# Kernel tuning notes

Measured on AMD Instinct MI355X. Metric: run time of the kernel, lower is better.

Reference implementation:

```python
import jax, jax.numpy as jnp
import numpy as np

NU, NI, K, D, B = 100000, 50000, 100, 64, 8192


def setup_inputs() -> dict:
    key = jax.random.key(0)
    ks = jax.random.split(key, 16)
    s = lambda fan_in: np.sqrt(2.0 / fan_in)  # kaiming_normal-ish scale
    return {
        "user_emb": jax.random.normal(ks[0], (NU, D), jnp.float32) * s(D),
        "item_emb": jax.random.normal(ks[1], (NI, D), jnp.float32) * s(D),
        "user_scr_tensor": jax.random.uniform(ks[2], (NU, K), jnp.float32) / K,
        "item_scr_tensor": jax.random.uniform(ks[3], (NI, K), jnp.float32) / K,
        "w1": jax.random.normal(ks[4], (64, 128), jnp.float32) * s(128),
        "b1": jnp.zeros((64,), jnp.float32),
        "w2": jax.random.normal(ks[5], (64, 64), jnp.float32) * s(64),
        "b2": jnp.zeros((64,), jnp.float32),
        "w3": jax.random.normal(ks[6], (32, 64), jnp.float32) * s(64),
        "b3": jnp.zeros((32,), jnp.float32),
        "w4": jax.random.normal(ks[7], (32, 32), jnp.float32) * s(32),
        "b4": jnp.zeros((32,), jnp.float32),
        "w5": jax.random.normal(ks[8], (1, 32), jnp.float32) * s(32),
        "b5": jnp.zeros((1,), jnp.float32),
        "user_idx_tensor": jax.random.randint(ks[9], (NU, K), 0, NU, jnp.int32),
        "item_idx_tensor": jax.random.randint(ks[10], (NI, K), 0, NI, jnp.int32),
        "user_idxs": jax.random.randint(ks[11], (B,), 0, NU, jnp.int32),
        "item_idxs": jax.random.randint(ks[12], (B,), 0, NI, jnp.int32),
    }


def _scored_pool(idx_tensor, emb, scr, idxs):
    neighs = idx_tensor[idxs]          # [B, K]
    neigh_emb = emb[neighs]            # [B, K, D]
    neigh_scr = scr[neighs]            # [B, K, K]
    return jnp.einsum("bkj,bjd->bkd", neigh_scr, neigh_emb)


def reference(user_emb, item_emb, user_scr_tensor, item_scr_tensor,
              w1, b1, w2, b2, w3, b3, w4, b4, w5, b5,
              user_idx_tensor, item_idx_tensor, user_idxs, item_idxs):
    su = _scored_pool(user_idx_tensor, user_emb, user_scr_tensor, user_idxs)  # [B,K,D]
    si = _scored_pool(item_idx_tensor, item_emb, item_scr_tensor, item_idxs)  # [B,K,D]
    x = jnp.concatenate([su, si], axis=2)  # [B, K, 2D]
    x = jax.nn.relu(x @ w1.T + b1)
    x = jax.nn.relu(x @ w2.T + b2)
    x = jax.nn.relu(x @ w3.T + b3)
    x = jax.nn.relu(x @ w4.T + b4)
    x = jax.nn.sigmoid(x @ w5.T + b5)  # [B, K, 1]
    return jnp.mean(x, axis=-2).squeeze()  # [B]
```

## Files before the change

### kernel.cpp

```cpp
#include <hip/hip_runtime.h>
#include <hip/hip_bf16.h>
#include <math.h>

typedef __attribute__((ext_vector_type(8))) short short8;
typedef __attribute__((ext_vector_type(4))) float f32x4;

#define KN 100

#define W1_OFF 0
#define W2_OFF 8192
#define W3_OFF 12288
#define W4_OFF 14336
#define SCRU_OFF 16384
#define SCRI_OFF (SCRU_OFF + 100000 * 128)
#define EMBU_OFF (SCRI_OFF + 50000 * 128)
#define EMBI_OFF (EMBU_OFF + 100000 * 64)
#define NB_OFF   (EMBI_OFF + 50000 * 64)

#define ETU 0
#define ETI 8704
#define XU  17408
#define XI  8704
#define S_TOT 25472

__device__ __forceinline__ unsigned short f2bf(float f) {
  __hip_bfloat16 h = __float2bfloat16(f);
  return __builtin_bit_cast(unsigned short, h);
}

__device__ __forceinline__ void st8(unsigned short* d, float4 a, float4 b) {
  short8 h;
  h[0] = (short)f2bf(a.x); h[1] = (short)f2bf(a.y);
  h[2] = (short)f2bf(a.z); h[3] = (short)f2bf(a.w);
  h[4] = (short)f2bf(b.x); h[5] = (short)f2bf(b.y);
  h[6] = (short)f2bf(b.z); h[7] = (short)f2bf(b.w);
  *reinterpret_cast<short8*>(d) = h;
}

__global__ void prep(const float* __restrict__ w1, const float* __restrict__ w2,
                     const float* __restrict__ w3, const float* __restrict__ w4,
                     const float* __restrict__ uscr, const float* __restrict__ iscr,
                     const float* __restrict__ uemb, const float* __restrict__ iemb,
                     const int* __restrict__ uidx_t, const int* __restrict__ iidx_t,
                     const int* __restrict__ uidxs, const int* __restrict__ iidxs,
                     unsigned short* __restrict__ ws) {
  int t = blockIdx.x * 256 + threadIdx.x;
  if (t < 15360) {
    const float* src; int rel, o, i, kt, base;
    if (t < 8192)       { src = w1; rel = t;         o = rel >> 7; i = rel & 127; kt = 4; base = W1_OFF; }
    else if (t < 12288) { src = w2; rel = t - 8192;  o = rel >> 6; i = rel & 63;  kt = 2; base = W2_OFF; }
    else if (t < 14336) { src = w3; rel = t - 12288; o = rel >> 6; i = rel & 63;  kt = 2; base = W3_OFF; }
    else                { src = w4; rel = t - 14336; o = rel >> 5; i = rel & 31;  kt = 1; base = W4_OFF; }
    int n = o >> 4, l15 = o & 15, k = i >> 5, quad = (i >> 3) & 3, j = i & 7;
    ws[base + ((n * kt + k) * 64 + quad * 16 + l15) * 8 + j] = f2bf(src[rel]);
    return;
  }
  int rel = t - 15360;
  const float4 z4 = {0.f, 0.f, 0.f, 0.f};
  if (rel < 2400000) {
    const float* src; unsigned short* dst; int row, g;
    if (rel < 1600000) {
      row = rel >> 4; g = rel & 15;
      src = uscr + (size_t)row * 100;
      dst = ws + SCRU_OFF + (size_t)row * 128 + g * 8;
    } else {
      int q = rel - 1600000; row = q >> 4; g = q & 15;
      src = iscr + (size_t)row * 100;
      dst = ws + SCRI_OFF + (size_t)row * 128 + g * 8;
    }
    float4 va = (g < 13) ? *reinterpret_cast<const float4*>(src + g * 8) : z4;
    float4 vb = (g < 12) ? *reinterpret_cast<const float4*>(src + g * 8 + 4) : z4;
    st8(dst, va, vb);
    return;
  }
  rel -= 2400000;
  if (rel < 1200000) {
    const float* src; unsigned short* dst; int row, g;
    if (rel < 800000) {
      row = rel >> 3; g = rel & 7;
      src = uemb + (size_t)row * 64;
      dst = ws + EMBU_OFF + (size_t)row * 64 + g * 8;
    } else {
      int q = rel - 800000; row = q >> 3; g = q & 7;
      src = iemb + (size_t)row * 64;
      dst = ws + EMBI_OFF + (size_t)row * 64 + g * 8;
    }
    float4 va = *reinterpret_cast<const float4*>(src + g * 8);
    float4 vb = *reinterpret_cast<const float4*>(src + g * 8 + 4);
    st8(dst, va, vb);
    return;
  }
  rel -= 1200000;
  if (rel < 2097152) {
    const int b = rel >> 8, i = rel & 255;
    int v;
    if (i < 128) {
      v = (i < KN) ? uidx_t[(size_t)uidxs[b] * KN + i] : 0;
    } else {
      const int j = i - 128;
      v = (j < KN) ? iidx_t[(size_t)iidxs[b] * KN + j] : 0;
    }
    ((int*)(ws + NB_OFF))[rel] = v;
  }
}

template <int NT, int KT>
__device__ __forceinline__ void mlp_layer(const short8* a,
                                          const unsigned short* __restrict__ gw,
                                          const float* __restrict__ bias,
                                          unsigned short* __restrict__ Y,
                                          int w, int l15, int quad, int lane) {
#pragma unroll
  for (int n = 0; n < NT; ++n) {
    f32x4 acc = {0.f, 0.f, 0.f, 0.f};
#pragma unroll
    for (int k = 0; k < KT; ++k) {
      short8 bf = *reinterpret_cast<const short8*>(gw + ((n * KT + k) * 64 + lane) * 8);
      acc = __builtin_amdgcn_mfma_f32_16x16x32_bf16(a[k], bf, acc, 0, 0, 0);
    }
    const int col = n * 16 + l15;
    const float bv = bias[col];
#pragma unroll
    for (int r = 0; r < 4; ++r) {
      float v = fmaxf(acc[r] + bv, 0.f);
      Y[(w * 16 + quad * 4 + r) * 72 + col] = f2bf(v);
    }
  }
}

__launch_bounds__(448, 6)
__global__ void cnn_mfma5(
    const unsigned short* __restrict__ ws,
    const float* __restrict__ b1, const float* __restrict__ b2,
    const float* __restrict__ b3, const float* __restrict__ b4,
    const float* __restrict__ w5, const float* __restrict__ b5,
    float* __restrict__ out) {
  __shared__ __align__(16) unsigned short S[S_TOT];
  __shared__ float s_red[7];

  const int b = blockIdx.x;
  const int tid = threadIdx.x;
  const int w = tid >> 6;
  const int lane = tid & 63;
  const int l15 = lane & 15, quad = lane >> 4;
  const int c = lane & 31, half = lane >> 5;

  const int* nbu = (const int*)(ws + NB_OFF) + (size_t)b * 256;
  const int* nbi = nbu + 128;
  const char* scru = (const char*)(ws + SCRU_OFF);
  const char* scri = (const char*)(ws + SCRI_OFF);
  const char* embu = (const char*)(ws + EMBU_OFF);
  const char* embi = (const char*)(ws + EMBI_OFF);

  const int mu = nbu[w * 16 + l15];
  const int mi = nbi[w * 16 + l15];

  short8 au[4], ai[4];
#pragma unroll
  for (int k = 0; k < 4; ++k)
    au[k] = *reinterpret_cast<const short8*>(scru + ((size_t)(unsigned)mu << 8) + k * 64 + quad * 16);
#pragma unroll
  for (int k = 0; k < 4; ++k)
    ai[k] = *reinterpret_cast<const short8*>(scri + ((size_t)(unsigned)mi << 8) + k * 64 + quad * 16);

  unsigned int du[8], di[8];
  int rv[8];
#pragma unroll
  for (int rr = 0; rr < 8; ++rr) {
    const int rbase = w + rr * 7;
    if (rbase < 50) {
      const int r = rbase * 2 + half;
      rv[rr] = r;
      du[rr] = *reinterpret_cast<const unsigned int*>(
          embu + ((size_t)(unsigned)nbu[r] << 7) + c * 4);
      di[rr] = *reinterpret_cast<const unsigned int*>(
          embi + ((size_t)(unsigned)nbi[r] << 7) + c * 4);
    }
  }
  for (int q = tid; q < 1792; q += 448) {
    const int buf = q / 896, rem = q - buf * 896;
    const int row = rem / 14, cp = rem - row * 14;
    *reinterpret_cast<unsigned int*>(&S[buf * 8704 + row * 136 + 100 + cp * 2]) = 0u;
  }
#pragma unroll
  for (int rr = 0; rr < 8; ++rr) {
    const int rbase = w + rr * 7;
    if (rbase < 50) {
      const int r = rv[rr];
      S[ETU + (2 * c) * 136 + r] = (unsigned short)(du[rr] & 0xffffu);
      S[ETU + (2 * c + 1) * 136 + r] = (unsigned short)(du[rr] >> 16);
      S[ETI + (2 * c) * 136 + r] = (unsigned short)(di[rr] & 0xffffu);
      S[ETI + (2 * c + 1) * 136 + r] = (unsigned short)(di[rr] >> 16);
    }
  }
  __syncthreads();

#pragma unroll
  for (int nt = 0; nt < 4; ++nt) {
    f32x4 acc = {0.f, 0.f, 0.f, 0.f};
#pragma unroll
    for (int kt = 0; kt < 4; ++kt) {
      short8 bf = *reinterpret_cast<const short8*>(
          S + ETU + (nt * 16 + l15) * 136 + kt * 32 + quad * 8);
      acc = __builtin_amdgcn_mfma_f32_16x16x32_bf16(au[kt], bf, acc, 0, 0, 0);
    }
#pragma unroll
    for (int r = 0; r < 4; ++r)
      S[XU + (w * 16 + quad * 4 + r) * 72 + nt * 16 + l15] = f2bf(acc[r]);
  }

  f32x4 acci[4];
#pragma unroll
  for (int nt = 0; nt < 4; ++nt) {
    f32x4 acc = {0.f, 0.f, 0.f, 0.f};
#pragma unroll
    for (int kt = 0; kt < 4; ++kt) {
      short8 bf = *reinterpret_cast<const short8*>(
          S + ETI + (nt * 16 + l15) * 136 + kt * 32 + quad * 8);
      acc = __builtin_amdgcn_mfma_f32_16x16x32_bf16(ai[kt], bf, acc, 0, 0, 0);
    }
    acci[nt] = acc;
  }
  __syncthreads();

#pragma unroll
  for (int nt = 0; nt < 4; ++nt)
#pragma unroll
    for (int r = 0; r < 4; ++r)
      S[XI + (w * 16 + quad * 4 + r) * 72 + nt * 16 + l15] = f2bf(acci[nt][r]);

  const unsigned short* xu_row = S + XU + (w * 16 + l15) * 72;
  const unsigned short* xi_row = S + XI + (w * 16 + l15) * 72;
  {
    short8 a[4];
    a[0] = *reinterpret_cast<const short8*>(xu_row + quad * 8);
    a[1] = *reinterpret_cast<const short8*>(xu_row + 32 + quad * 8);
    a[2] = *reinterpret_cast<const short8*>(xi_row + quad * 8);
    a[3] = *reinterpret_cast<const short8*>(xi_row + 32 + quad * 8);
    mlp_layer<4, 4>(a, ws + W1_OFF, b1, S + XU, w, l15, quad, lane);
  }
  {
    short8 a[2];
    a[0] = *reinterpret_cast<const short8*>(xu_row + quad * 8);
    a[1] = *reinterpret_cast<const short8*>(xu_row + 32 + quad * 8);
    mlp_layer<4, 2>(a, ws + W2_OFF, b2, S + XI, w, l15, quad, lane);
  }
  {
    short8 a[2];
    a[0] = *reinterpret_cast<const short8*>(xi_row + quad * 8);
    a[1] = *reinterpret_cast<const short8*>(xi_row + 32 + quad * 8);
    mlp_layer<2, 2>(a, ws + W3_OFF, b3, S + XU, w, l15, quad, lane);
  }
  {
    short8 a = *reinterpret_cast<const short8*>(xu_row + quad * 8);
    float dot[4] = {0.f, 0.f, 0.f, 0.f};
#pragma unroll
    for (int n = 0; n < 2; ++n) {
      f32x4 acc = {0.f, 0.f, 0.f, 0.f};
      short8 bf = *reinterpret_cast<const short8*>(ws + W4_OFF + (n * 64 + lane) * 8);
      acc = __builtin_amdgcn_mfma_f32_16x16x32_bf16(a, bf, acc, 0, 0, 0);
      const int col = n * 16 + l15;
      const float bv = b4[col], wv = w5[col];
#pragma unroll
      for (int r = 0; r < 4; ++r) {
        float v = fmaxf(acc[r] + bv, 0.f);
        dot[r] = fmaf(v, wv, dot[r]);
      }
    }
    float wsum = 0.f;
    const float bb5 = b5[0];
#pragma unroll
    for (int r = 0; r < 4; ++r) {
      float s = dot[r];
      s += __shfl_xor(s, 1, 64);
      s += __shfl_xor(s, 2, 64);
      s += __shfl_xor(s, 4, 64);
      s += __shfl_xor(s, 8, 64);
      const int row = w * 16 + quad * 4 + r;
      if (l15 == 0 && row < KN) wsum += 1.f / (1.f + expf(-(s + bb5)));
    }
    wsum += __shfl_xor(wsum, 16, 64);
    wsum += __shfl_xor(wsum, 32, 64);
    if (lane == 0) s_red[w] = wsum;
  }
  __syncthreads();
  if (tid == 0) {
    float t = 0.f;
#pragma unroll
    for (int i = 0; i < 7; ++i) t += s_red[i];
    out[b] = t * (1.0f / KN);
  }
}

extern "C" void kernel_launch(void* const* d_in, const int* in_sizes, int n_in,
                              void* d_out, int out_size, void* d_ws,
                              size_t ws_size, hipStream_t stream) {
  const float* user_emb = (const float*)d_in[0];
  const float* item_emb = (const float*)d_in[1];
  const float* user_scr = (const float*)d_in[2];
  const float* item_scr = (const float*)d_in[3];
  const float* w1 = (const float*)d_in[4];
  const float* b1 = (const float*)d_in[5];
  const float* w2 = (const float*)d_in[6];
  const float* b2 = (const float*)d_in[7];
  const float* w3 = (const float*)d_in[8];
  const float* b3 = (const float*)d_in[9];
  const float* w4 = (const float*)d_in[10];
  const float* b4 = (const float*)d_in[11];
  const float* w5 = (const float*)d_in[12];
  const float* b5 = (const float*)d_in[13];
  const int* user_idx_t = (const int*)d_in[14];
  const int* item_idx_t = (const int*)d_in[15];
  const int* user_idxs = (const int*)d_in[16];
  const int* item_idxs = (const int*)d_in[17];
  unsigned short* wsw = (unsigned short*)d_ws;

  const int prep_threads = 15360 + 2400000 + 1200000 + 2097152;
  prep<<<dim3((prep_threads + 255) / 256), dim3(256), 0, stream>>>(
      w1, w2, w3, w4, user_scr, item_scr, user_emb, item_emb,
      user_idx_t, item_idx_t, user_idxs, item_idxs, wsw);

  const int B = in_sizes[16];
  cnn_mfma5<<<dim3(B), dim3(448), 0, stream>>>(
      wsw, b1, b2, b3, b4, w5, b5, (float*)d_out);
}
```

Before: 401.6 us.

## Process eight batch rows per block with software-pipelined neighbor gathers

The main kernel now handles eight batch elements per block in a loop and double-buffers the transposed embedding tiles in shared memory. The next element's score and embedding gathers are issued while the current element's pooling MFMAs run. Neighbor index lookup moves out of the prep kernel into the main kernel and is prefetched one step ahead, and embedding transposes use packed 32-bit LDS stores built with a cross-half shuffle. The cost is more LDS per block, a lower occupancy hint (4 instead of 6), fewer blocks (B/8), and B must be divisible by 8.

```diff
diff --git a/kernel.cpp b/kernel.cpp
--- a/kernel.cpp
+++ b/kernel.cpp
@@ -6,6 +6,7 @@
 typedef __attribute__((ext_vector_type(4))) float f32x4;
 
 #define KN 100
+#define NBP 8
 
 #define W1_OFF 0
 #define W2_OFF 8192
@@ -15,13 +16,12 @@
 #define SCRI_OFF (SCRU_OFF + 100000 * 128)
 #define EMBU_OFF (SCRI_OFF + 50000 * 128)
 #define EMBI_OFF (EMBU_OFF + 100000 * 64)
-#define NB_OFF   (EMBI_OFF + 50000 * 64)
-
-#define ETU 0
-#define ETI 8704
-#define XU  17408
-#define XI  8704
-#define S_TOT 25472
+
+#define ETB0 0
+#define ETB1 8704
+#define XU   17408
+#define XI   25472
+#define S_TOT 33536
 
 __device__ __forceinline__ unsigned short f2bf(float f) {
   __hip_bfloat16 h = __float2bfloat16(f);
@@ -41,8 +41,6 @@
                      const float* __restrict__ w3, const float* __restrict__ w4,
                      const float* __restrict__ uscr, const float* __restrict__ iscr,
                      const float* __restrict__ uemb, const float* __restrict__ iemb,
-                     const int* __restrict__ uidx_t, const int* __restrict__ iidx_t,
-                     const int* __restrict__ uidxs, const int* __restrict__ iidxs,
                      unsigned short* __restrict__ ws) {
   int t = blockIdx.x * 256 + threadIdx.x;
   if (t < 15360) {
@@ -88,19 +86,6 @@
     float4 va = *reinterpret_cast<const float4*>(src + g * 8);
     float4 vb = *reinterpret_cast<const float4*>(src + g * 8 + 4);
     st8(dst, va, vb);
-    return;
-  }
-  rel -= 1200000;
-  if (rel < 2097152) {
-    const int b = rel >> 8, i = rel & 255;
-    int v;
-    if (i < 128) {
-      v = (i < KN) ? uidx_t[(size_t)uidxs[b] * KN + i] : 0;
-    } else {
-      const int j = i - 128;
-      v = (j < KN) ? iidx_t[(size_t)iidxs[b] * KN + j] : 0;
-    }
-    ((int*)(ws + NB_OFF))[rel] = v;
   }
 }
 
@@ -128,167 +113,232 @@
   }
 }
 
-__launch_bounds__(448, 6)
-__global__ void cnn_mfma5(
+__device__ __forceinline__ void et_pack_store(unsigned short* S, int etb,
+                                              unsigned int v, int c, int half,
+                                              int rbase) {
+  unsigned int pv = (unsigned int)__shfl_xor((int)v, 32, 64);
+  unsigned int packed = (half == 0) ? ((v & 0xffffu) | (pv << 16))
+                                    : ((pv >> 16) | (v & 0xffff0000u));
+  *reinterpret_cast<unsigned int*>(&S[etb + (2 * c + half) * 136 + 2 * rbase]) = packed;
+}
+
+__launch_bounds__(448, 4)
+__global__ void cnn_mfma6(
     const unsigned short* __restrict__ ws,
     const float* __restrict__ b1, const float* __restrict__ b2,
     const float* __restrict__ b3, const float* __restrict__ b4,
     const float* __restrict__ w5, const float* __restrict__ b5,
+    const int* __restrict__ uidx_t, const int* __restrict__ iidx_t,
+    const int* __restrict__ uidxs, const int* __restrict__ iidxs,
     float* __restrict__ out) {
   __shared__ __align__(16) unsigned short S[S_TOT];
-  __shared__ float s_red[7];
-
-  const int b = blockIdx.x;
+  __shared__ int s_nb[2][256];
+  __shared__ float s_red[NBP][7];
+
+  const int b0 = blockIdx.x * NBP;
   const int tid = threadIdx.x;
-  const int w = tid >> 6;
-  const int lane = tid & 63;
+  const int w = tid >> 6, lane = tid & 63;
   const int l15 = lane & 15, quad = lane >> 4;
   const int c = lane & 31, half = lane >> 5;
 
-  const int* nbu = (const int*)(ws + NB_OFF) + (size_t)b * 256;
-  const int* nbi = nbu + 128;
   const char* scru = (const char*)(ws + SCRU_OFF);
   const char* scri = (const char*)(ws + SCRI_OFF);
   const char* embu = (const char*)(ws + EMBU_OFF);
   const char* embi = (const char*)(ws + EMBI_OFF);
 
-  const int mu = nbu[w * 16 + l15];
-  const int mi = nbi[w * 16 + l15];
-
-  short8 au[4], ai[4];
-#pragma unroll
-  for (int k = 0; k < 4; ++k)
-    au[k] = *reinterpret_cast<const short8*>(scru + ((size_t)(unsigned)mu << 8) + k * 64 + quad * 16);
-#pragma unroll
-  for (int k = 0; k < 4; ++k)
-    ai[k] = *reinterpret_cast<const short8*>(scri + ((size_t)(unsigned)mi << 8) + k * 64 + quad * 16);
-
-  unsigned int du[8], di[8];
-  int rv[8];
+  for (int q = tid; q < 1792; q += 448) {
+    const int buf = q / 896, rem = q - buf * 896;
+    const int row = rem / 14, cp = rem - row * 14;
+    *reinterpret_cast<unsigned int*>(&S[buf * 8704 + row * 136 + 100 + cp * 2]) = 0u;
+  }
+
+  int nbreg = 0;
+  if (tid < 256) {
+    const int col = tid & 127;
+    const bool isu = tid < 128;
+    const int* idx_t = isu ? uidx_t : iidx_t;
+    int h0 = isu ? uidxs[b0] : iidxs[b0];
+    s_nb[0][tid] = (col < KN) ? idx_t[(size_t)h0 * KN + col] : 0;
+    int h1 = isu ? uidxs[b0 + 1] : iidxs[b0 + 1];
+    nbreg = (col < KN) ? idx_t[(size_t)h1 * KN + col] : 0;
+  }
+  __syncthreads();
+
+  short8 a_cur[4];
+  {
+    const int m = s_nb[0][w * 16 + l15];
+#pragma unroll
+    for (int k = 0; k < 4; ++k)
+      a_cur[k] = *reinterpret_cast<const short8*>(
+          scru + ((size_t)(unsigned)m << 8) + k * 64 + quad * 16);
+  }
 #pragma unroll
   for (int rr = 0; rr < 8; ++rr) {
     const int rbase = w + rr * 7;
     if (rbase < 50) {
       const int r = rbase * 2 + half;
-      rv[rr] = r;
-      du[rr] = *reinterpret_cast<const unsigned int*>(
-          embu + ((size_t)(unsigned)nbu[r] << 7) + c * 4);
-      di[rr] = *reinterpret_cast<const unsigned int*>(
-          embi + ((size_t)(unsigned)nbi[r] << 7) + c * 4);
-    }
-  }
-  for (int q = tid; q < 1792; q += 448) {
-    const int buf = q / 896, rem = q - buf * 896;
-    const int row = rem / 14, cp = rem - row * 14;
-    *reinterpret_cast<unsigned int*>(&S[buf * 8704 + row * 136 + 100 + cp * 2]) = 0u;
-  }
-#pragma unroll
-  for (int rr = 0; rr < 8; ++rr) {
-    const int rbase = w + rr * 7;
-    if (rbase < 50) {
-      const int r = rv[rr];
-      S[ETU + (2 * c) * 136 + r] = (unsigned short)(du[rr] & 0xffffu);
-      S[ETU + (2 * c + 1) * 136 + r] = (unsigned short)(du[rr] >> 16);
-      S[ETI + (2 * c) * 136 + r] = (unsigned short)(di[rr] & 0xffffu);
-      S[ETI + (2 * c + 1) * 136 + r] = (unsigned short)(di[rr] >> 16);
+      unsigned int v = *reinterpret_cast<const unsigned int*>(
+          embu + ((size_t)(unsigned)s_nb[0][r] << 7) + c * 4);
+      et_pack_store(S, ETB0, v, c, half, rbase);
     }
   }
   __syncthreads();
 
-#pragma unroll
-  for (int nt = 0; nt < 4; ++nt) {
-    f32x4 acc = {0.f, 0.f, 0.f, 0.f};
-#pragma unroll
-    for (int kt = 0; kt < 4; ++kt) {
-      short8 bf = *reinterpret_cast<const short8*>(
-          S + ETU + (nt * 16 + l15) * 136 + kt * 32 + quad * 8);
-      acc = __builtin_amdgcn_mfma_f32_16x16x32_bf16(au[kt], bf, acc, 0, 0, 0);
-    }
-#pragma unroll
-    for (int r = 0; r < 4; ++r)
-      S[XU + (w * 16 + quad * 4 + r) * 72 + nt * 16 + l15] = f2bf(acc[r]);
-  }
-
-  f32x4 acci[4];
-#pragma unroll
-  for (int nt = 0; nt < 4; ++nt) {
-    f32x4 acc = {0.f, 0.f, 0.f, 0.f};
-#pragma unroll
-    for (int kt = 0; kt < 4; ++kt) {
-      short8 bf = *reinterpret_cast<const short8*>(
-          S + ETI + (nt * 16 + l15) * 136 + kt * 32 + quad * 8);
-      acc = __builtin_amdgcn_mfma_f32_16x16x32_bf16(ai[kt], bf, acc, 0, 0, 0);
-    }
-    acci[nt] = acc;
-  }
-  __syncthreads();
-
-#pragma unroll
-  for (int nt = 0; nt < 4; ++nt)
-#pragma unroll
-    for (int r = 0; r < 4; ++r)
-      S[XI + (w * 16 + quad * 4 + r) * 72 + nt * 16 + l15] = f2bf(acci[nt][r]);
-
-  const unsigned short* xu_row = S + XU + (w * 16 + l15) * 72;
-  const unsigned short* xi_row = S + XI + (w * 16 + l15) * 72;
-  {
-    short8 a[4];
-    a[0] = *reinterpret_cast<const short8*>(xu_row + quad * 8);
-    a[1] = *reinterpret_cast<const short8*>(xu_row + 32 + quad * 8);
-    a[2] = *reinterpret_cast<const short8*>(xi_row + quad * 8);
-    a[3] = *reinterpret_cast<const short8*>(xi_row + 32 + quad * 8);
-    mlp_layer<4, 4>(a, ws + W1_OFF, b1, S + XU, w, l15, quad, lane);
-  }
-  {
-    short8 a[2];
-    a[0] = *reinterpret_cast<const short8*>(xu_row + quad * 8);
-    a[1] = *reinterpret_cast<const short8*>(xu_row + 32 + quad * 8);
-    mlp_layer<4, 2>(a, ws + W2_OFF, b2, S + XI, w, l15, quad, lane);
-  }
-  {
-    short8 a[2];
-    a[0] = *reinterpret_cast<const short8*>(xi_row + quad * 8);
-    a[1] = *reinterpret_cast<const short8*>(xi_row + 32 + quad * 8);
-    mlp_layer<2, 2>(a, ws + W3_OFF, b3, S + XU, w, l15, quad, lane);
-  }
-  {
-    short8 a = *reinterpret_cast<const short8*>(xu_row + quad * 8);
-    float dot[4] = {0.f, 0.f, 0.f, 0.f};
-#pragma unroll
-    for (int n = 0; n < 2; ++n) {
+#pragma unroll 1
+  for (int b = 0; b < NBP; ++b) {
+    const int cur = b & 1, nxt = cur ^ 1;
+
+    short8 a_nx[4];
+    {
+      const int m = s_nb[cur][128 + w * 16 + l15];
+#pragma unroll
+      for (int k = 0; k < 4; ++k)
+        a_nx[k] = *reinterpret_cast<const short8*>(
+            scri + ((size_t)(unsigned)m << 8) + k * 64 + quad * 16);
+    }
+    unsigned int etv[8];
+#pragma unroll
+    for (int rr = 0; rr < 8; ++rr) {
+      const int rbase = w + rr * 7;
+      if (rbase < 50) {
+        const int r = rbase * 2 + half;
+        etv[rr] = *reinterpret_cast<const unsigned int*>(
+            embi + ((size_t)(unsigned)s_nb[cur][128 + r] << 7) + c * 4);
+      }
+    }
+#pragma unroll
+    for (int nt = 0; nt < 4; ++nt) {
       f32x4 acc = {0.f, 0.f, 0.f, 0.f};
-      short8 bf = *reinterpret_cast<const short8*>(ws + W4_OFF + (n * 64 + lane) * 8);
-      acc = __builtin_amdgcn_mfma_f32_16x16x32_bf16(a, bf, acc, 0, 0, 0);
-      const int col = n * 16 + l15;
-      const float bv = b4[col], wv = w5[col];
+#pragma unroll
+      for (int kt = 0; kt < 4; ++kt) {
+        short8 bf = *reinterpret_cast<const short8*>(
+            S + ETB0 + (nt * 16 + l15) * 136 + kt * 32 + quad * 8);
+        acc = __builtin_amdgcn_mfma_f32_16x16x32_bf16(a_cur[kt], bf, acc, 0, 0, 0);
+      }
+#pragma unroll
+      for (int r = 0; r < 4; ++r)
+        S[XU + (w * 16 + quad * 4 + r) * 72 + nt * 16 + l15] = f2bf(acc[r]);
+    }
+    if (tid < 256 && b + 1 < NBP) s_nb[nxt][tid] = nbreg;
+#pragma unroll
+    for (int rr = 0; rr < 8; ++rr) {
+      const int rbase = w + rr * 7;
+      if (rbase < 50) et_pack_store(S, ETB1, etv[rr], c, half, rbase);
+    }
+#pragma unroll
+    for (int k = 0; k < 4; ++k) a_cur[k] = a_nx[k];
+    __syncthreads();
+
+    if (tid < 256 && b + 2 < NBP) {
+      const int col = tid & 127;
+      const bool isu = tid < 128;
+      const int* idx_t = isu ? uidx_t : iidx_t;
+      int h = isu ? uidxs[b0 + b + 2] : iidxs[b0 + b + 2];
+      nbreg = (col < KN) ? idx_t[(size_t)h * KN + col] : 0;
+    }
+    short8 a_nu[4];
+    unsigned int etu[8];
+    if (b + 1 < NBP) {
+      const int m = s_nb[nxt][w * 16 + l15];
+#pragma unroll
+      for (int k = 0; k < 4; ++k)
+        a_nu[k] = *reinterpret_cast<const short8*>(
+            scru + ((size_t)(unsigned)m << 8) + k * 64 + quad * 16);
+#pragma unroll
+      for (int rr = 0; rr < 8; ++rr) {
+        const int rbase = w + rr * 7;
+        if (rbase < 50) {
+          const int r = rbase * 2 + half;
+          etu[rr] = *reinterpret_cast<const unsigned int*>(
+              embu + ((size_t)(unsigned)s_nb[nxt][r] << 7) + c * 4);
+        }
+      }
+    }
+#pragma unroll
+    for (int nt = 0; nt < 4; ++nt) {
+      f32x4 acc = {0.f, 0.f, 0.f, 0.f};
+#pragma unroll
+      for (int kt = 0; kt < 4; ++kt) {
+        short8 bf = *reinterpret_cast<const short8*>(
+            S + ETB1 + (nt * 16 + l15) * 136 + kt * 32 + quad * 8);
+        acc = __builtin_amdgcn_mfma_f32_16x16x32_bf16(a_cur[kt], bf, acc, 0, 0, 0);
+      }
+#pragma unroll
+      for (int r = 0; r < 4; ++r)
+        S[XI + (w * 16 + quad * 4 + r) * 72 + nt * 16 + l15] = f2bf(acc[r]);
+    }
+    if (b + 1 < NBP) {
+#pragma unroll
+      for (int rr = 0; rr < 8; ++rr) {
+        const int rbase = w + rr * 7;
+        if (rbase < 50) et_pack_store(S, ETB0, etu[rr], c, half, rbase);
+      }
+#pragma unroll
+      for (int k = 0; k < 4; ++k) a_cur[k] = a_nu[k];
+    }
+
+    const unsigned short* xu_row = S + XU + (w * 16 + l15) * 72;
+    const unsigned short* xi_row = S + XI + (w * 16 + l15) * 72;
+    {
+      short8 a[4];
+      a[0] = *reinterpret_cast<const short8*>(xu_row + quad * 8);
+      a[1] = *reinterpret_cast<const short8*>(xu_row + 32 + quad * 8);
+      a[2] = *reinterpret_cast<const short8*>(xi_row + quad * 8);
+      a[3] = *reinterpret_cast<const short8*>(xi_row + 32 + quad * 8);
+      mlp_layer<4, 4>(a, ws + W1_OFF, b1, S + XU, w, l15, quad, lane);
+    }
+    {
+      short8 a[2];
+      a[0] = *reinterpret_cast<const short8*>(xu_row + quad * 8);
+      a[1] = *reinterpret_cast<const short8*>(xu_row + 32 + quad * 8);
+      mlp_layer<4, 2>(a, ws + W2_OFF, b2, S + XI, w, l15, quad, lane);
+    }
+    {
+      short8 a[2];
+      a[0] = *reinterpret_cast<const short8*>(xi_row + quad * 8);
+      a[1] = *reinterpret_cast<const short8*>(xi_row + 32 + quad * 8);
+      mlp_layer<2, 2>(a, ws + W3_OFF, b3, S + XU, w, l15, quad, lane);
+    }
+    {
+      short8 a = *reinterpret_cast<const short8*>(xu_row + quad * 8);
+      float dot[4] = {0.f, 0.f, 0.f, 0.f};
+#pragma unroll
+      for (int n = 0; n < 2; ++n) {
+        f32x4 acc = {0.f, 0.f, 0.f, 0.f};
+        short8 bf = *reinterpret_cast<const short8*>(ws + W4_OFF + (n * 64 + lane) * 8);
+        acc = __builtin_amdgcn_mfma_f32_16x16x32_bf16(a, bf, acc, 0, 0, 0);
+        const int col = n * 16 + l15;
+        const float bv = b4[col], wv = w5[col];
+#pragma unroll
+        for (int r = 0; r < 4; ++r) {
+          float v = fmaxf(acc[r] + bv, 0.f);
+          dot[r] = fmaf(v, wv, dot[r]);
+        }
+      }
+      float wsum = 0.f;
+      const float bb5 = b5[0];
 #pragma unroll
       for (int r = 0; r < 4; ++r) {
-        float v = fmaxf(acc[r] + bv, 0.f);
-        dot[r] = fmaf(v, wv, dot[r]);
-      }
-    }
-    float wsum = 0.f;
-    const float bb5 = b5[0];
-#pragma unroll
-    for (int r = 0; r < 4; ++r) {
-      float s = dot[r];
-      s += __shfl_xor(s, 1, 64);
-      s += __shfl_xor(s, 2, 64);
-      s += __shfl_xor(s, 4, 64);
-      s += __shfl_xor(s, 8, 64);
-      const int row = w * 16 + quad * 4 + r;
-      if (l15 == 0 && row < KN) wsum += 1.f / (1.f + expf(-(s + bb5)));
-    }
-    wsum += __shfl_xor(wsum, 16, 64);
-    wsum += __shfl_xor(wsum, 32, 64);
-    if (lane == 0) s_red[w] = wsum;
-  }
-  __syncthreads();
-  if (tid == 0) {
+        float s = dot[r];
+        s += __shfl_xor(s, 1, 64);
+        s += __shfl_xor(s, 2, 64);
+        s += __shfl_xor(s, 4, 64);
+        s += __shfl_xor(s, 8, 64);
+        const int row = w * 16 + quad * 4 + r;
+        if (l15 == 0 && row < KN) wsum += 1.f / (1.f + expf(-(s + bb5)));
+      }
+      wsum += __shfl_xor(wsum, 16, 64);
+      wsum += __shfl_xor(wsum, 32, 64);
+      if (lane == 0) s_red[b][w] = wsum;
+    }
+    __syncthreads();
+  }
+
+  if (tid < NBP) {
     float t = 0.f;
 #pragma unroll
-    for (int i = 0; i < 7; ++i) t += s_red[i];
-    out[b] = t * (1.0f / KN);
+    for (int i = 0; i < 7; ++i) t += s_red[tid][i];
+    out[b0 + tid] = t * (1.0f / KN);
   }
 }
 
@@ -315,12 +365,11 @@
   const int* item_idxs = (const int*)d_in[17];
   unsigned short* wsw = (unsigned short*)d_ws;
 
-  const int prep_threads = 15360 + 2400000 + 1200000 + 2097152;
-  prep<<<dim3((prep_threads + 255) / 256), dim3(256), 0, stream>>>(
-      w1, w2, w3, w4, user_scr, item_scr, user_emb, item_emb,
-      user_idx_t, item_idx_t, user_idxs, item_idxs, wsw);
+  prep<<<dim3((15360 + 2400000 + 1200000 + 255) / 256), dim3(256), 0, stream>>>(
+      w1, w2, w3, w4, user_scr, item_scr, user_emb, item_emb, wsw);
 
   const int B = in_sizes[16];
-  cnn_mfma5<<<dim3(B), dim3(448), 0, stream>>>(
-      wsw, b1, b2, b3, b4, w5, b5, (float*)d_out);
-}
+  cnn_mfma6<<<dim3(B / NBP), dim3(448), 0, stream>>>(
+      wsw, b1, b2, b3, b4, w5, b5, user_idx_t, item_idx_t, user_idxs,
+      item_idxs, (float*)d_out);
+}
```

New measurement: 624.5 us. +55.5%, slower.
